# Kernel tuning notes

Hardware: AMD Instinct MI355X
Metric: run time of the kernel (lower is better)

## Reference

```python
import jax, jax.numpy as jnp
import numpy as np

D_MODEL, D_K, D_V, N_HEADS = 1024, 64, 64, 16
LN_EPS = 1e-5
NEG = -1e9

def setup_inputs() -> dict:
    key = jax.random.key(0)
    ks = jax.random.split(key, 8)
    B, S = 2, 2048
    inp = {
        'input_Q': jax.random.normal(ks[0], (B, S, D_MODEL), jnp.float32),
        'input_K': jax.random.normal(ks[1], (B, S, D_MODEL), jnp.float32),
        'input_V': jax.random.normal(ks[2], (B, S, D_MODEL), jnp.float32),
        'attn_mask': jax.random.randint(ks[3], (B, S, S), 0, 2).astype(bool),
    }
    sc = 1.0 / np.sqrt(D_MODEL)
    # weights stored as [in, out] so application is x @ W (matches torch Linear math)
    inp['W_Q'] = jax.random.uniform(ks[4], (D_MODEL, N_HEADS * D_K), jnp.float32, -sc, sc)
    inp['W_K'] = jax.random.uniform(ks[5], (D_MODEL, N_HEADS * D_K), jnp.float32, -sc, sc)
    inp['W_V'] = jax.random.uniform(ks[6], (D_MODEL, N_HEADS * D_V), jnp.float32, -sc, sc)
    inp['W_O'] = jax.random.uniform(ks[7], (N_HEADS * D_V, D_MODEL), jnp.float32, -sc, sc)
    return inp

def _mha(input_Q, input_K, input_V, attn_mask, W_Q, W_K, W_V, W_O):
    B, S, _ = input_Q.shape
    Q = (input_Q @ W_Q).reshape(B, S, N_HEADS, D_K).transpose(0, 2, 1, 3)  # [B,H,S,dk]
    K = (input_K @ W_K).reshape(B, S, N_HEADS, D_K).transpose(0, 2, 1, 3)
    V = (input_V @ W_V).reshape(B, S, N_HEADS, D_V).transpose(0, 2, 1, 3)
    scores = jnp.einsum('bhqd,bhkd->bhqk', Q, K) / np.sqrt(D_K)
    scores = jnp.where(attn_mask[:, None, :, :], NEG, scores)
    attn = jax.nn.softmax(scores, axis=-1)  # [B,H,S,S]
    context = jnp.einsum('bhqk,bhkd->bhqd', attn, V)
    context = context.transpose(0, 2, 1, 3).reshape(B, S, N_HEADS * D_V)
    output = context @ W_O
    y = output + input_Q  # residual
    # LayerNorm created fresh in forward: gamma=1, beta=0, eps=1e-5
    mu = jnp.mean(y, axis=-1, keepdims=True)
    var = jnp.mean((y - mu) ** 2, axis=-1, keepdims=True)
    out = (y - mu) / jnp.sqrt(var + LN_EPS)
    return out, attn

def reference(input_Q, input_K, input_V, attn_mask, W_Q, W_K, W_V, W_O):
    return _mha(input_Q, input_K, input_V, attn_mask, W_Q, W_K, W_V, W_O)
```

## Files before the change

### kernel.cpp

```cpp
#include <hip/hip_runtime.h>
#include <hip/hip_bf16.h>

typedef __attribute__((ext_vector_type(8))) short bf16x8;
typedef __attribute__((ext_vector_type(4))) float f32x4;

#define S 2048
#define DM 1024
#define NH 16
#define B_ 2

struct __align__(8) us4 { unsigned short a, b, c, d; };

static __device__ __forceinline__ unsigned short f2bf(float f) {
  unsigned int u = __builtin_bit_cast(unsigned int, f);
  u += 0x7fffu + ((u >> 16) & 1u);
  return (unsigned short)(u >> 16);
}

__global__ __launch_bounds__(256) void k_cvt(const float* __restrict__ x,
                                             unsigned short* __restrict__ y, int n) {
  int i = (blockIdx.x * 256 + threadIdx.x) * 4;
  if (i >= n) return;
  float4 v = *(const float4*)(x + i);
  us4 o; o.a = f2bf(v.x); o.b = f2bf(v.y); o.c = f2bf(v.z); o.d = f2bf(v.w);
  *(us4*)(y + i) = o;
}

__global__ __launch_bounds__(256) void k_wtr(const float* __restrict__ W,
                                             unsigned short* __restrict__ Wt) {
  __shared__ float tile[32][33];
  int n0 = blockIdx.x * 32, k0 = blockIdx.y * 32;
  int t = threadIdx.x;
  int r = t >> 3, c = (t & 7) * 4;
  float4 v = *(const float4*)(W + (long)(k0 + r) * DM + n0 + c);
  tile[r][c] = v.x; tile[r][c + 1] = v.y; tile[r][c + 2] = v.z; tile[r][c + 3] = v.w;
  __syncthreads();
  us4 o;
  o.a = f2bf(tile[c][r]); o.b = f2bf(tile[c + 1][r]);
  o.c = f2bf(tile[c + 2][r]); o.d = f2bf(tile[c + 3][r]);
  *(us4*)(Wt + (long)(n0 + r) * DM + k0 + c) = o;
}

template <int F32OUT>
__global__ __launch_bounds__(256) void k_gemm_nt(const unsigned short* __restrict__ A,
                                                 const unsigned short* __restrict__ Bt,
                                                 unsigned short* __restrict__ Cb,
                                                 float* __restrict__ Cf,
                                                 int M, int N, int K) {
  __shared__ unsigned short sA[128 * 40];
  __shared__ unsigned short sB[128 * 40];
  int t = threadIdx.x;
  int wave = t >> 6, lane = t & 63, quad = lane >> 4, l16 = lane & 15;
  int wm = (wave >> 1) * 64, wn = (wave & 1) * 64;
  long m0 = (long)blockIdx.x * 128, n0 = (long)blockIdx.y * 128;
  f32x4 acc[4][4] = {};
  int srow = t >> 1, sc = (t & 1) * 16;
  const unsigned short* Ag = A + (m0 + srow) * K + sc;
  const unsigned short* Bg = Bt + (n0 + srow) * K + sc;
  unsigned short* sAp = sA + srow * 40 + sc;
  unsigned short* sBp = sB + srow * 40 + sc;
  for (int k0 = 0; k0 < K; k0 += 32) {
    __syncthreads();
    int4 a0 = *(const int4*)(Ag + k0);
    int4 a1 = *(const int4*)(Ag + k0 + 8);
    int4 b0 = *(const int4*)(Bg + k0);
    int4 b1 = *(const int4*)(Bg + k0 + 8);
    *(int4*)(sAp) = a0; *(int4*)(sAp + 8) = a1;
    *(int4*)(sBp) = b0; *(int4*)(sBp + 8) = b1;
    __syncthreads();
    bf16x8 af[4], bfr[4];
#pragma unroll
    for (int i = 0; i < 4; i++) af[i] = *(const bf16x8*)(sA + (wm + i * 16 + l16) * 40 + quad * 8);
#pragma unroll
    for (int j = 0; j < 4; j++) bfr[j] = *(const bf16x8*)(sB + (wn + j * 16 + l16) * 40 + quad * 8);
#pragma unroll
    for (int i = 0; i < 4; i++)
#pragma unroll
      for (int j = 0; j < 4; j++)
        acc[i][j] = __builtin_amdgcn_mfma_f32_16x16x32_bf16(af[i], bfr[j], acc[i][j], 0, 0, 0);
  }
#pragma unroll
  for (int i = 0; i < 4; i++)
#pragma unroll
    for (int j = 0; j < 4; j++)
#pragma unroll
      for (int r = 0; r < 4; r++) {
        long row = m0 + wm + i * 16 + quad * 4 + r;
        long col = n0 + wn + j * 16 + l16;
        float v = acc[i][j][r];
        if (F32OUT) Cf[row * N + col] = v;
        else Cb[row * N + col] = f2bf(v);
      }
}

__global__ __launch_bounds__(256) void k_vtr(const unsigned short* __restrict__ Vp,
                                             unsigned short* __restrict__ Vt) {
  __shared__ unsigned short tile[64][72];
  int b = blockIdx.z, h = blockIdx.y, s0 = blockIdx.x * 64;
  int t = threadIdx.x;
  int r = t >> 2, c = (t & 3) * 16;
  const unsigned short* src = Vp + (long)(b * S + s0 + r) * DM + h * 64;
  *(int4*)(&tile[r][c]) = *(const int4*)(src + c);
  *(int4*)(&tile[r][c + 8]) = *(const int4*)(src + c + 8);
  __syncthreads();
  unsigned short o[16] __attribute__((aligned(16)));
#pragma unroll
  for (int i = 0; i < 16; i++) o[i] = tile[c + i][r];
  unsigned short* dst = Vt + ((long)(b * NH + h) * 64 + r) * S + s0 + c;
  *(int4*)(dst) = *(int4*)(o);
  *(int4*)(dst + 8) = *(int4*)(o + 8);
}

__global__ __launch_bounds__(256) void k_attn(const unsigned short* __restrict__ Qb,
                                              const unsigned short* __restrict__ Kb,
                                              const unsigned short* __restrict__ Vt,
                                              const int* __restrict__ mask,
                                              float* __restrict__ attn,
                                              unsigned short* __restrict__ ctx) {
  __shared__ unsigned short sQ[16 * 72];
  __shared__ unsigned short sK[128 * 72];
  __shared__ float sP[16 * 132];
  __shared__ float red[4][16];
  __shared__ float linv[16];
  int b = blockIdx.z, h = blockIdx.y, q0 = blockIdx.x * 16;
  int t = threadIdx.x;
  int wave = t >> 6, lane = t & 63, quad = lane >> 4, l16 = lane & 15;
  {
    int r = t >> 4, c = (t & 15) * 4;
    *(uint2*)(sQ + r * 72 + c) =
        *(const uint2*)(Qb + (long)(b * S + q0 + r) * DM + h * 64 + c);
  }
  const long mbase = (long)b * S * S;
  int krow = t >> 1, kc0 = (t & 1) * 32;
  const unsigned short* Kg = Kb + (long)(b * S + krow) * DM + h * 64 + kc0;
  unsigned short* sKp = sK + krow * 72 + kc0;

  float lsum[4] = {0.f, 0.f, 0.f, 0.f};
  for (int kt = 0; kt < 16; kt++) {
    __syncthreads();
    {
      const unsigned short* g = Kg + (long)kt * 128 * DM;
      *(int4*)(sKp) = *(const int4*)(g);
      *(int4*)(sKp + 8) = *(const int4*)(g + 8);
      *(int4*)(sKp + 16) = *(const int4*)(g + 16);
      *(int4*)(sKp + 24) = *(const int4*)(g + 24);
    }
    __syncthreads();
    bf16x8 aq0 = *(const bf16x8*)(sQ + l16 * 72 + quad * 8);
    bf16x8 aq1 = *(const bf16x8*)(sQ + l16 * 72 + 32 + quad * 8);
#pragma unroll
    for (int j = 0; j < 2; j++) {
      int kl = wave * 32 + j * 16 + l16;
      bf16x8 bk0 = *(const bf16x8*)(sK + kl * 72 + quad * 8);
      bf16x8 bk1 = *(const bf16x8*)(sK + kl * 72 + 32 + quad * 8);
      f32x4 fa = {0.f, 0.f, 0.f, 0.f};
      fa = __builtin_amdgcn_mfma_f32_16x16x32_bf16(aq0, bk0, fa, 0, 0, 0);
      fa = __builtin_amdgcn_mfma_f32_16x16x32_bf16(aq1, bk1, fa, 0, 0, 0);
      int colg = kt * 128 + kl;
#pragma unroll
      for (int r = 0; r < 4; r++) {
        int rowg = q0 + quad * 4 + r;
        int m = mask[mbase + (long)rowg * S + colg];
        float p = m ? 0.f : __expf(fa[r] * 0.125f);
        lsum[r] += p;
      }
    }
  }
#pragma unroll
  for (int r = 0; r < 4; r++)
    for (int off = 1; off < 16; off <<= 1) lsum[r] += __shfl_xor(lsum[r], off, 64);
  if (l16 == 0)
#pragma unroll
    for (int r = 0; r < 4; r++) red[wave][quad * 4 + r] = lsum[r];
  __syncthreads();
  if (t < 16) linv[t] = 1.f / (red[0][t] + red[1][t] + red[2][t] + red[3][t]);

  f32x4 oacc = {0.f, 0.f, 0.f, 0.f};
  const unsigned short* vbase = Vt + ((long)(b * NH + h) * 64 + wave * 16 + l16) * S;
  for (int kt = 0; kt < 16; kt++) {
    __syncthreads();
    {
      const unsigned short* g = Kg + (long)kt * 128 * DM;
      *(int4*)(sKp) = *(const int4*)(g);
      *(int4*)(sKp + 8) = *(const int4*)(g + 8);
      *(int4*)(sKp + 16) = *(const int4*)(g + 16);
      *(int4*)(sKp + 24) = *(const int4*)(g + 24);
    }
    __syncthreads();
    bf16x8 aq0 = *(const bf16x8*)(sQ + l16 * 72 + quad * 8);
    bf16x8 aq1 = *(const bf16x8*)(sQ + l16 * 72 + 32 + quad * 8);
#pragma unroll
    for (int j = 0; j < 2; j++) {
      int kl = wave * 32 + j * 16 + l16;
      bf16x8 bk0 = *(const bf16x8*)(sK + kl * 72 + quad * 8);
      bf16x8 bk1 = *(const bf16x8*)(sK + kl * 72 + 32 + quad * 8);
      f32x4 fa = {0.f, 0.f, 0.f, 0.f};
      fa = __builtin_amdgcn_mfma_f32_16x16x32_bf16(aq0, bk0, fa, 0, 0, 0);
      fa = __builtin_amdgcn_mfma_f32_16x16x32_bf16(aq1, bk1, fa, 0, 0, 0);
      int colg = kt * 128 + kl;
#pragma unroll
      for (int r = 0; r < 4; r++) {
        int rowg = q0 + quad * 4 + r;
        int m = mask[mbase + (long)rowg * S + colg];
        float p = m ? 0.f : __expf(fa[r] * 0.125f);
        sP[(quad * 4 + r) * 132 + wave * 32 + j * 16 + l16] = p;
      }
    }
    __syncthreads();
    {
      int r = t >> 4, c = (t & 15) * 8;
      float li = linv[r];
      const float* sp = sP + r * 132 + c;
      float4 v0 = *(const float4*)(sp);
      float4 v1 = *(const float4*)(sp + 4);
      v0.x *= li; v0.y *= li; v0.z *= li; v0.w *= li;
      v1.x *= li; v1.y *= li; v1.z *= li; v1.w *= li;
      float* dst = attn + ((long)(b * NH + h) * S + q0 + r) * S + kt * 128 + c;
      *(float4*)(dst) = v0;
      *(float4*)(dst + 4) = v1;
    }
#pragma unroll
    for (int ks = 0; ks < 4; ks++) {
      const float* ap = sP + l16 * 132 + ks * 32 + quad * 8;
      float4 a0 = *(const float4*)(ap);
      float4 a1 = *(const float4*)(ap + 4);
      bf16x8 a8;
      a8[0] = (short)f2bf(a0.x); a8[1] = (short)f2bf(a0.y);
      a8[2] = (short)f2bf(a0.z); a8[3] = (short)f2bf(a0.w);
      a8[4] = (short)f2bf(a1.x); a8[5] = (short)f2bf(a1.y);
      a8[6] = (short)f2bf(a1.z); a8[7] = (short)f2bf(a1.w);
      bf16x8 v8 = *(const bf16x8*)(vbase + kt * 128 + ks * 32 + quad * 8);
      oacc = __builtin_amdgcn_mfma_f32_16x16x32_bf16(a8, v8, oacc, 0, 0, 0);
    }
  }
#pragma unroll
  for (int r = 0; r < 4; r++) {
    int rowg = q0 + quad * 4 + r;
    float v = oacc[r] * linv[quad * 4 + r];
    ctx[((long)(b * S + rowg) * NH + h) * 64 + wave * 16 + l16] = f2bf(v);
  }
}

__global__ __launch_bounds__(256) void k_ln(const float* __restrict__ Y,
                                            const float* __restrict__ X,
                                            float* __restrict__ out) {
  __shared__ float rs[4], rs2[4];
  long row = blockIdx.x;
  int t = threadIdx.x;
  float4 v = *(const float4*)(Y + row * DM + t * 4);
  float4 xv = *(const float4*)(X + row * DM + t * 4);
  v.x += xv.x; v.y += xv.y; v.z += xv.z; v.w += xv.w;
  float s = v.x + v.y + v.z + v.w;
  float s2 = v.x * v.x + v.y * v.y + v.z * v.z + v.w * v.w;
  for (int off = 1; off < 64; off <<= 1) {
    s += __shfl_xor(s, off, 64);
    s2 += __shfl_xor(s2, off, 64);
  }
  int wave = t >> 6;
  if ((t & 63) == 0) { rs[wave] = s; rs2[wave] = s2; }
  __syncthreads();
  s = rs[0] + rs[1] + rs[2] + rs[3];
  s2 = rs2[0] + rs2[1] + rs2[2] + rs2[3];
  float mu = s * (1.f / 1024.f);
  float var = s2 * (1.f / 1024.f) - mu * mu;
  float rstd = rsqrtf(var + 1e-5f);
  float4 o;
  o.x = (v.x - mu) * rstd; o.y = (v.y - mu) * rstd;
  o.z = (v.z - mu) * rstd; o.w = (v.w - mu) * rstd;
  *(float4*)(out + row * DM + t * 4) = o;
}

extern "C" void kernel_launch(void* const* d_in, const int* in_sizes, int n_in,
                              void* d_out, int out_size, void* d_ws, size_t ws_size,
                              hipStream_t stream) {
  const float* inQ = (const float*)d_in[0];
  const float* inK = (const float*)d_in[1];
  const float* inV = (const float*)d_in[2];
  const int* mask = (const int*)d_in[3];
  const float* WQ = (const float*)d_in[4];
  const float* WK = (const float*)d_in[5];
  const float* WV = (const float*)d_in[6];
  const float* WO = (const float*)d_in[7];
  float* out = (float*)d_out;
  float* attn = out + (long)B_ * S * DM;

  char* ws = (char*)d_ws;
  const size_t MB = 1048576;
  unsigned short* WtQ = (unsigned short*)(ws + 0 * MB);
  unsigned short* WtK = (unsigned short*)(ws + 2 * MB);
  unsigned short* WtV = (unsigned short*)(ws + 4 * MB);
  unsigned short* WtO = (unsigned short*)(ws + 6 * MB);
  unsigned short* Xq = (unsigned short*)(ws + 8 * MB);
  unsigned short* Xk = (unsigned short*)(ws + 16 * MB);
  unsigned short* Xv = (unsigned short*)(ws + 24 * MB);
  unsigned short* Qb = (unsigned short*)(ws + 32 * MB);
  unsigned short* Kbf = (unsigned short*)(ws + 40 * MB);
  unsigned short* Vp = (unsigned short*)(ws + 48 * MB);
  unsigned short* Vtr = (unsigned short*)(ws + 56 * MB);
  unsigned short* ctx = (unsigned short*)(ws + 24 * MB);
  float* Yf = (float*)(ws + 8 * MB);

  dim3 blk(256);
  int n = B_ * S * DM;

  k_wtr<<<dim3(32, 32), blk, 0, stream>>>(WQ, WtQ);
  k_wtr<<<dim3(32, 32), blk, 0, stream>>>(WK, WtK);
  k_wtr<<<dim3(32, 32), blk, 0, stream>>>(WV, WtV);
  k_wtr<<<dim3(32, 32), blk, 0, stream>>>(WO, WtO);
  k_cvt<<<n / 1024, blk, 0, stream>>>(inQ, Xq, n);
  k_cvt<<<n / 1024, blk, 0, stream>>>(inK, Xk, n);
  k_cvt<<<n / 1024, blk, 0, stream>>>(inV, Xv, n);

  k_gemm_nt<0><<<dim3(32, 8), blk, 0, stream>>>(Xq, WtQ, Qb, nullptr, 4096, 1024, 1024);
  k_gemm_nt<0><<<dim3(32, 8), blk, 0, stream>>>(Xk, WtK, Kbf, nullptr, 4096, 1024, 1024);
  k_gemm_nt<0><<<dim3(32, 8), blk, 0, stream>>>(Xv, WtV, Vp, nullptr, 4096, 1024, 1024);

  k_vtr<<<dim3(32, 16, 2), blk, 0, stream>>>(Vp, Vtr);

  k_attn<<<dim3(128, 16, 2), blk, 0, stream>>>(Qb, Kbf, Vtr, mask, attn, ctx);

  k_gemm_nt<1><<<dim3(32, 8), blk, 0, stream>>>(ctx, WtO, nullptr, Yf, 4096, 1024, 1024);

  k_ln<<<B_ * S, blk, 0, stream>>>(Yf, inQ, out);
}
```

Before: 1.012 ms.

## Split attention into flash-style context kernel and tiled score-writer with bit-packed mask

Replaces the per-16-row attention kernel, which recomputed QK^T twice and read the int mask twice, with two kernels. A flash-style kernel accumulates row sums and P·V over 128-row query tiles and stores the inverse row sums. A separate 128x128 tiled kernel then recomputes the scores and writes the normalized attention matrix. The mask is first packed into bits with a ballot so the attention kernels read far less mask data. The GEMMs are also rewritten to use direct global-to-LDS loads with XOR swizzling, a K-step of 64 and 128x64 tiles. This adds a mask-packing pass and reuses workspace regions, which relies on the order of the stream.

```diff
diff --git a/kernel.cpp b/kernel.cpp
--- a/kernel.cpp
+++ b/kernel.cpp
@@ -15,6 +15,12 @@
   unsigned int u = __builtin_bit_cast(unsigned int, f);
   u += 0x7fffu + ((u >> 16) & 1u);
   return (unsigned short)(u >> 16);
+}
+
+typedef __attribute__((address_space(3))) unsigned int lds_u32;
+typedef __attribute__((address_space(1))) unsigned int gbl_u32;
+static __device__ __forceinline__ void gl_lds16(const unsigned short* g, short* l) {
+  __builtin_amdgcn_global_load_lds((gbl_u32*)(void*)g, (lds_u32*)l, 16, 0, 0);
 }
 
 __global__ __launch_bounds__(256) void k_cvt(const float* __restrict__ x,
@@ -41,48 +47,65 @@
   *(us4*)(Wt + (long)(n0 + r) * DM + k0 + c) = o;
 }
 
+__global__ __launch_bounds__(256) void k_pack(const int* __restrict__ mask,
+                                              unsigned int* __restrict__ bits) {
+  long gid = (long)blockIdx.x * 256 + threadIdx.x;
+  int m = mask[gid];
+  unsigned long long bm = __ballot(m != 0);
+  if ((threadIdx.x & 63) == 0) *(unsigned long long*)(bits + (gid >> 5)) = bm;
+}
+
 template <int F32OUT>
-__global__ __launch_bounds__(256) void k_gemm_nt(const unsigned short* __restrict__ A,
-                                                 const unsigned short* __restrict__ Bt,
-                                                 unsigned short* __restrict__ Cb,
-                                                 float* __restrict__ Cf,
-                                                 int M, int N, int K) {
-  __shared__ unsigned short sA[128 * 40];
-  __shared__ unsigned short sB[128 * 40];
+__global__ __launch_bounds__(256) void k_gemm2(const unsigned short* __restrict__ A,
+                                               const unsigned short* __restrict__ Bt,
+                                               unsigned short* __restrict__ Cb,
+                                               float* __restrict__ Cf,
+                                               int M, int N, int K) {
+  __shared__ __align__(16) char smem[24576];
+  short* sA = (short*)smem;
+  short* sB = (short*)(smem + 16384);
   int t = threadIdx.x;
   int wave = t >> 6, lane = t & 63, quad = lane >> 4, l16 = lane & 15;
-  int wm = (wave >> 1) * 64, wn = (wave & 1) * 64;
-  long m0 = (long)blockIdx.x * 128, n0 = (long)blockIdx.y * 128;
-  f32x4 acc[4][4] = {};
-  int srow = t >> 1, sc = (t & 1) * 16;
-  const unsigned short* Ag = A + (m0 + srow) * K + sc;
-  const unsigned short* Bg = Bt + (n0 + srow) * K + sc;
-  unsigned short* sAp = sA + srow * 40 + sc;
-  unsigned short* sBp = sB + srow * 40 + sc;
-  for (int k0 = 0; k0 < K; k0 += 32) {
+  int wm = (wave >> 1) * 64, wn = (wave & 1) * 32;
+  long m0 = (long)blockIdx.x * 128, n0 = (long)blockIdx.y * 64;
+  f32x4 acc[4][2] = {};
+  for (int k0 = 0; k0 < K; k0 += 64) {
     __syncthreads();
-    int4 a0 = *(const int4*)(Ag + k0);
-    int4 a1 = *(const int4*)(Ag + k0 + 8);
-    int4 b0 = *(const int4*)(Bg + k0);
-    int4 b1 = *(const int4*)(Bg + k0 + 8);
-    *(int4*)(sAp) = a0; *(int4*)(sAp + 8) = a1;
-    *(int4*)(sBp) = b0; *(int4*)(sBp + 8) = b1;
+#pragma unroll
+    for (int rr = 0; rr < 6; rr++) {
+      int id = rr * 4 + wave;
+      if (id < 16) {
+        int flat = id * 64 + lane;
+        int row = flat >> 3, cp = flat & 7, sw = cp ^ (row & 7);
+        gl_lds16(A + (m0 + row) * K + k0 + sw * 8, sA + id * 512);
+      } else {
+        int c = id - 16;
+        int flat = c * 64 + lane;
+        int row = flat >> 3, cp = flat & 7, sw = cp ^ (row & 7);
+        gl_lds16(Bt + (n0 + row) * K + k0 + sw * 8, sB + c * 512);
+      }
+    }
     __syncthreads();
-    bf16x8 af[4], bfr[4];
-#pragma unroll
-    for (int i = 0; i < 4; i++) af[i] = *(const bf16x8*)(sA + (wm + i * 16 + l16) * 40 + quad * 8);
-#pragma unroll
-    for (int j = 0; j < 4; j++) bfr[j] = *(const bf16x8*)(sB + (wn + j * 16 + l16) * 40 + quad * 8);
-#pragma unroll
-    for (int i = 0; i < 4; i++)
-#pragma unroll
-      for (int j = 0; j < 4; j++)
-        acc[i][j] = __builtin_amdgcn_mfma_f32_16x16x32_bf16(af[i], bfr[j], acc[i][j], 0, 0, 0);
+#pragma unroll
+    for (int kk = 0; kk < 2; kk++) {
+      bf16x8 af[4], bf_[2];
+#pragma unroll
+      for (int i = 0; i < 4; i++)
+        af[i] = *(const bf16x8*)(sA + (wm + i * 16 + l16) * 64 + (((kk * 4 + quad) ^ (l16 & 7)) * 8));
+#pragma unroll
+      for (int j = 0; j < 2; j++)
+        bf_[j] = *(const bf16x8*)(sB + (wn + j * 16 + l16) * 64 + (((kk * 4 + quad) ^ (l16 & 7)) * 8));
+#pragma unroll
+      for (int i = 0; i < 4; i++)
+#pragma unroll
+        for (int j = 0; j < 2; j++)
+          acc[i][j] = __builtin_amdgcn_mfma_f32_16x16x32_bf16(af[i], bf_[j], acc[i][j], 0, 0, 0);
+    }
   }
 #pragma unroll
   for (int i = 0; i < 4; i++)
 #pragma unroll
-    for (int j = 0; j < 4; j++)
+    for (int j = 0; j < 2; j++)
 #pragma unroll
       for (int r = 0; r < 4; r++) {
         long row = m0 + wm + i * 16 + quad * 4 + r;
@@ -111,134 +134,208 @@
   *(int4*)(dst + 8) = *(int4*)(o + 8);
 }
 
-__global__ __launch_bounds__(256) void k_attn(const unsigned short* __restrict__ Qb,
-                                              const unsigned short* __restrict__ Kb,
-                                              const unsigned short* __restrict__ Vt,
-                                              const int* __restrict__ mask,
-                                              float* __restrict__ attn,
-                                              unsigned short* __restrict__ ctx) {
-  __shared__ unsigned short sQ[16 * 72];
-  __shared__ unsigned short sK[128 * 72];
-  __shared__ float sP[16 * 132];
-  __shared__ float red[4][16];
-  __shared__ float linv[16];
-  int b = blockIdx.z, h = blockIdx.y, q0 = blockIdx.x * 16;
+__global__ __launch_bounds__(256) void k_flash(const unsigned short* __restrict__ Qb,
+                                               const unsigned short* __restrict__ Kb,
+                                               const unsigned short* __restrict__ Vt,
+                                               const unsigned int* __restrict__ mbits,
+                                               float* __restrict__ linvG,
+                                               unsigned short* __restrict__ ctx) {
+  __shared__ __align__(16) char smem[52736];
+  short* sP = (short*)smem;
+  short* sQ = (short*)(smem + 18432);
+  short* sK = (short*)(smem + 18432 + 16384);
+  short* sV = (short*)(smem + 18432 + 16384 + 8192);
+  unsigned long long* sM = (unsigned long long*)(smem + 18432 + 16384 + 8192 + 8192);
+  float* sLi = (float*)(smem + 18432 + 16384 + 8192 + 8192 + 1024);
+
+  const int b = blockIdx.z, h = blockIdx.y, q0 = blockIdx.x * 128;
+  const int bh = b * NH + h;
+  const int t = threadIdx.x;
+  const int wave = t >> 6, lane = t & 63, quad = lane >> 4, l16 = lane & 15;
+
+#pragma unroll
+  for (int rr = 0; rr < 4; rr++) {
+    int c = rr * 4 + wave;
+    int flat = c * 64 + lane;
+    int row = flat >> 3, cp = flat & 7, sw = cp ^ (row & 7);
+    gl_lds16(Qb + (long)(b * S + q0 + row) * DM + h * 64 + sw * 8, sQ + c * 512);
+  }
+  __syncthreads();
+  bf16x8 aq[2][2];
+#pragma unroll
+  for (int i = 0; i < 2; i++)
+#pragma unroll
+    for (int kk = 0; kk < 2; kk++)
+      aq[i][kk] = *(const bf16x8*)(sQ + (wave * 32 + i * 16 + l16) * 64 +
+                                   (((kk * 4 + quad) ^ (l16 & 7)) * 8));
+
+  f32x4 oacc[2][4] = {};
+  float lsum[2][4] = {};
+
+  for (int kt = 0; kt < 32; kt++) {
+    __syncthreads();
+#pragma unroll
+    for (int rr = 0; rr < 4; rr++) {
+      int id = rr * 4 + wave;
+      if (id < 8) {
+        int flat = id * 64 + lane;
+        int row = flat >> 3, cp = flat & 7, sw = cp ^ (row & 7);
+        gl_lds16(Kb + (long)(b * S + kt * 64 + row) * DM + h * 64 + sw * 8, sK + id * 512);
+      } else {
+        int cc = id - 8;
+        int flat = cc * 64 + lane;
+        int d = flat >> 3, cp = flat & 7, sw = cp ^ (d & 7);
+        gl_lds16(Vt + (long)(bh * 64 + d) * S + kt * 64 + sw * 8, sV + cc * 512);
+      }
+    }
+    if (t < 128)
+      sM[t] = *(const unsigned long long*)(mbits + ((long)(b * S) + q0 + t) * 64 + kt * 2);
+    __syncthreads();
+    f32x4 sacc[2][4] = {};
+#pragma unroll
+    for (int kk = 0; kk < 2; kk++) {
+      bf16x8 bk[4];
+#pragma unroll
+      for (int j = 0; j < 4; j++)
+        bk[j] = *(const bf16x8*)(sK + (j * 16 + l16) * 64 + (((kk * 4 + quad) ^ (l16 & 7)) * 8));
+#pragma unroll
+      for (int i = 0; i < 2; i++)
+#pragma unroll
+        for (int j = 0; j < 4; j++)
+          sacc[i][j] = __builtin_amdgcn_mfma_f32_16x16x32_bf16(aq[i][kk], bk[j], sacc[i][j], 0, 0, 0);
+    }
+#pragma unroll
+    for (int i = 0; i < 2; i++)
+#pragma unroll
+      for (int r = 0; r < 4; r++) {
+        int rl = wave * 32 + i * 16 + quad * 4 + r;
+        unsigned long long mw = sM[rl];
+        float ls = 0.f;
+#pragma unroll
+        for (int j = 0; j < 4; j++) {
+          int cb = j * 16 + l16;
+          float p = ((mw >> cb) & 1ull) ? 0.f : __expf(sacc[i][j][r] * 0.125f);
+          ls += p;
+          sP[rl * 72 + cb] = (short)f2bf(p);
+        }
+        lsum[i][r] += ls;
+      }
+    __syncthreads();
+#pragma unroll
+    for (int ks = 0; ks < 2; ks++) {
+      bf16x8 aP[2], bV[4];
+#pragma unroll
+      for (int i = 0; i < 2; i++)
+        aP[i] = *(const bf16x8*)(sP + (wave * 32 + i * 16 + l16) * 72 + ks * 32 + quad * 8);
+#pragma unroll
+      for (int j = 0; j < 4; j++)
+        bV[j] = *(const bf16x8*)(sV + (j * 16 + l16) * 64 + (((ks * 4 + quad) ^ (l16 & 7)) * 8));
+#pragma unroll
+      for (int i = 0; i < 2; i++)
+#pragma unroll
+        for (int j = 0; j < 4; j++)
+          oacc[i][j] = __builtin_amdgcn_mfma_f32_16x16x32_bf16(aP[i], bV[j], oacc[i][j], 0, 0, 0);
+    }
+  }
+#pragma unroll
+  for (int i = 0; i < 2; i++)
+#pragma unroll
+    for (int r = 0; r < 4; r++) {
+      float v = lsum[i][r];
+      for (int off = 1; off < 16; off <<= 1) v += __shfl_xor(v, off, 64);
+      if (l16 == 0) {
+        int rl = wave * 32 + i * 16 + quad * 4 + r;
+        float li = 1.f / v;
+        sLi[rl] = li;
+        linvG[(long)bh * S + q0 + rl] = li;
+      }
+    }
+  __syncthreads();
+#pragma unroll
+  for (int i = 0; i < 2; i++)
+#pragma unroll
+    for (int r = 0; r < 4; r++) {
+      int rl = wave * 32 + i * 16 + quad * 4 + r;
+      float li = sLi[rl];
+#pragma unroll
+      for (int j = 0; j < 4; j++) {
+        float v = oacc[i][j][r] * li;
+        ctx[((long)(b * S + q0 + rl) * NH + h) * 64 + j * 16 + l16] = f2bf(v);
+      }
+    }
+}
+
+__global__ __launch_bounds__(256) void k_score(const unsigned short* __restrict__ Qb,
+                                               const unsigned short* __restrict__ Kb,
+                                               const unsigned int* __restrict__ mbits,
+                                               const float* __restrict__ linvG,
+                                               float* __restrict__ attn) {
+  __shared__ __align__(16) char smem[35328];
+  short* sQ = (short*)smem;
+  short* sK = (short*)(smem + 16384);
+  unsigned long long* sM = (unsigned long long*)(smem + 32768);
+  float* sLi = (float*)(smem + 32768 + 2048);
+  int q0 = blockIdx.x * 128, k0 = blockIdx.y * 128, bh = blockIdx.z;
+  int b = bh >> 4, h = bh & 15;
   int t = threadIdx.x;
   int wave = t >> 6, lane = t & 63, quad = lane >> 4, l16 = lane & 15;
+  int wq = wave >> 1, wk = wave & 1;
+#pragma unroll
+  for (int rr = 0; rr < 8; rr++) {
+    int id = rr * 4 + wave;
+    if (id < 16) {
+      int flat = id * 64 + lane;
+      int row = flat >> 3, cp = flat & 7, sw = cp ^ (row & 7);
+      gl_lds16(Qb + (long)(b * S + q0 + row) * DM + h * 64 + sw * 8, sQ + id * 512);
+    } else {
+      int c = id - 16;
+      int flat = c * 64 + lane;
+      int row = flat >> 3, cp = flat & 7, sw = cp ^ (row & 7);
+      gl_lds16(Kb + (long)(b * S + k0 + row) * DM + h * 64 + sw * 8, sK + c * 512);
+    }
+  }
   {
-    int r = t >> 4, c = (t & 15) * 4;
-    *(uint2*)(sQ + r * 72 + c) =
-        *(const uint2*)(Qb + (long)(b * S + q0 + r) * DM + h * 64 + c);
-  }
-  const long mbase = (long)b * S * S;
-  int krow = t >> 1, kc0 = (t & 1) * 32;
-  const unsigned short* Kg = Kb + (long)(b * S + krow) * DM + h * 64 + kc0;
-  unsigned short* sKp = sK + krow * 72 + kc0;
-
-  float lsum[4] = {0.f, 0.f, 0.f, 0.f};
-  for (int kt = 0; kt < 16; kt++) {
-    __syncthreads();
-    {
-      const unsigned short* g = Kg + (long)kt * 128 * DM;
-      *(int4*)(sKp) = *(const int4*)(g);
-      *(int4*)(sKp + 8) = *(const int4*)(g + 8);
-      *(int4*)(sKp + 16) = *(const int4*)(g + 16);
-      *(int4*)(sKp + 24) = *(const int4*)(g + 24);
-    }
-    __syncthreads();
-    bf16x8 aq0 = *(const bf16x8*)(sQ + l16 * 72 + quad * 8);
-    bf16x8 aq1 = *(const bf16x8*)(sQ + l16 * 72 + 32 + quad * 8);
-#pragma unroll
-    for (int j = 0; j < 2; j++) {
-      int kl = wave * 32 + j * 16 + l16;
-      bf16x8 bk0 = *(const bf16x8*)(sK + kl * 72 + quad * 8);
-      bf16x8 bk1 = *(const bf16x8*)(sK + kl * 72 + 32 + quad * 8);
-      f32x4 fa = {0.f, 0.f, 0.f, 0.f};
-      fa = __builtin_amdgcn_mfma_f32_16x16x32_bf16(aq0, bk0, fa, 0, 0, 0);
-      fa = __builtin_amdgcn_mfma_f32_16x16x32_bf16(aq1, bk1, fa, 0, 0, 0);
-      int colg = kt * 128 + kl;
-#pragma unroll
-      for (int r = 0; r < 4; r++) {
-        int rowg = q0 + quad * 4 + r;
-        int m = mask[mbase + (long)rowg * S + colg];
-        float p = m ? 0.f : __expf(fa[r] * 0.125f);
-        lsum[r] += p;
-      }
-    }
-  }
-#pragma unroll
-  for (int r = 0; r < 4; r++)
-    for (int off = 1; off < 16; off <<= 1) lsum[r] += __shfl_xor(lsum[r], off, 64);
-  if (l16 == 0)
-#pragma unroll
-    for (int r = 0; r < 4; r++) red[wave][quad * 4 + r] = lsum[r];
-  __syncthreads();
-  if (t < 16) linv[t] = 1.f / (red[0][t] + red[1][t] + red[2][t] + red[3][t]);
-
-  f32x4 oacc = {0.f, 0.f, 0.f, 0.f};
-  const unsigned short* vbase = Vt + ((long)(b * NH + h) * 64 + wave * 16 + l16) * S;
-  for (int kt = 0; kt < 16; kt++) {
-    __syncthreads();
-    {
-      const unsigned short* g = Kg + (long)kt * 128 * DM;
-      *(int4*)(sKp) = *(const int4*)(g);
-      *(int4*)(sKp + 8) = *(const int4*)(g + 8);
-      *(int4*)(sKp + 16) = *(const int4*)(g + 16);
-      *(int4*)(sKp + 24) = *(const int4*)(g + 24);
-    }
-    __syncthreads();
-    bf16x8 aq0 = *(const bf16x8*)(sQ + l16 * 72 + quad * 8);
-    bf16x8 aq1 = *(const bf16x8*)(sQ + l16 * 72 + 32 + quad * 8);
-#pragma unroll
-    for (int j = 0; j < 2; j++) {
-      int kl = wave * 32 + j * 16 + l16;
-      bf16x8 bk0 = *(const bf16x8*)(sK + kl * 72 + quad * 8);
-      bf16x8 bk1 = *(const bf16x8*)(sK + kl * 72 + 32 + quad * 8);
-      f32x4 fa = {0.f, 0.f, 0.f, 0.f};
-      fa = __builtin_amdgcn_mfma_f32_16x16x32_bf16(aq0, bk0, fa, 0, 0, 0);
-      fa = __builtin_amdgcn_mfma_f32_16x16x32_bf16(aq1, bk1, fa, 0, 0, 0);
-      int colg = kt * 128 + kl;
-#pragma unroll
-      for (int r = 0; r < 4; r++) {
-        int rowg = q0 + quad * 4 + r;
-        int m = mask[mbase + (long)rowg * S + colg];
-        float p = m ? 0.f : __expf(fa[r] * 0.125f);
-        sP[(quad * 4 + r) * 132 + wave * 32 + j * 16 + l16] = p;
-      }
-    }
-    __syncthreads();
-    {
-      int r = t >> 4, c = (t & 15) * 8;
-      float li = linv[r];
-      const float* sp = sP + r * 132 + c;
-      float4 v0 = *(const float4*)(sp);
-      float4 v1 = *(const float4*)(sp + 4);
-      v0.x *= li; v0.y *= li; v0.z *= li; v0.w *= li;
-      v1.x *= li; v1.y *= li; v1.z *= li; v1.w *= li;
-      float* dst = attn + ((long)(b * NH + h) * S + q0 + r) * S + kt * 128 + c;
-      *(float4*)(dst) = v0;
-      *(float4*)(dst + 4) = v1;
-    }
-#pragma unroll
-    for (int ks = 0; ks < 4; ks++) {
-      const float* ap = sP + l16 * 132 + ks * 32 + quad * 8;
-      float4 a0 = *(const float4*)(ap);
-      float4 a1 = *(const float4*)(ap + 4);
-      bf16x8 a8;
-      a8[0] = (short)f2bf(a0.x); a8[1] = (short)f2bf(a0.y);
-      a8[2] = (short)f2bf(a0.z); a8[3] = (short)f2bf(a0.w);
-      a8[4] = (short)f2bf(a1.x); a8[5] = (short)f2bf(a1.y);
-      a8[6] = (short)f2bf(a1.z); a8[7] = (short)f2bf(a1.w);
-      bf16x8 v8 = *(const bf16x8*)(vbase + kt * 128 + ks * 32 + quad * 8);
-      oacc = __builtin_amdgcn_mfma_f32_16x16x32_bf16(a8, v8, oacc, 0, 0, 0);
-    }
-  }
-#pragma unroll
-  for (int r = 0; r < 4; r++) {
-    int rowg = q0 + quad * 4 + r;
-    float v = oacc[r] * linv[quad * 4 + r];
-    ctx[((long)(b * S + rowg) * NH + h) * 64 + wave * 16 + l16] = f2bf(v);
-  }
+    int row = t >> 1, half = t & 1;
+    sM[row * 2 + half] =
+        *(const unsigned long long*)(mbits + ((long)(b * S) + q0 + row) * 64 + (k0 >> 5) + half * 2);
+  }
+  if (t < 128) sLi[t] = linvG[(long)bh * S + q0 + t];
+  __syncthreads();
+  bf16x8 a_[4][2], b_[4][2];
+#pragma unroll
+  for (int i = 0; i < 4; i++)
+#pragma unroll
+    for (int kk = 0; kk < 2; kk++)
+      a_[i][kk] = *(const bf16x8*)(sQ + (wq * 64 + i * 16 + l16) * 64 +
+                                   (((kk * 4 + quad) ^ (l16 & 7)) * 8));
+#pragma unroll
+  for (int j = 0; j < 4; j++)
+#pragma unroll
+    for (int kk = 0; kk < 2; kk++)
+      b_[j][kk] = *(const bf16x8*)(sK + (wk * 64 + j * 16 + l16) * 64 +
+                                   (((kk * 4 + quad) ^ (l16 & 7)) * 8));
+  f32x4 sacc[4][4] = {};
+#pragma unroll
+  for (int kk = 0; kk < 2; kk++)
+#pragma unroll
+    for (int i = 0; i < 4; i++)
+#pragma unroll
+      for (int j = 0; j < 4; j++)
+        sacc[i][j] = __builtin_amdgcn_mfma_f32_16x16x32_bf16(a_[i][kk], b_[j][kk], sacc[i][j], 0, 0, 0);
+#pragma unroll
+  for (int i = 0; i < 4; i++)
+#pragma unroll
+    for (int r = 0; r < 4; r++) {
+      int rl = wq * 64 + i * 16 + quad * 4 + r;
+      unsigned long long mw = sM[rl * 2 + wk];
+      float li = sLi[rl];
+      float* dst = attn + ((long)bh * S + q0 + rl) * S + k0 + wk * 64;
+#pragma unroll
+      for (int j = 0; j < 4; j++) {
+        float p = ((mw >> (j * 16 + l16)) & 1ull) ? 0.f : __expf(sacc[i][j][r] * 0.125f) * li;
+        dst[j * 16 + l16] = p;
+      }
+    }
 }
 
 __global__ __launch_bounds__(256) void k_ln(const float* __restrict__ Y,
@@ -297,6 +394,8 @@
   unsigned short* Kbf = (unsigned short*)(ws + 40 * MB);
   unsigned short* Vp = (unsigned short*)(ws + 48 * MB);
   unsigned short* Vtr = (unsigned short*)(ws + 56 * MB);
+  unsigned int* mbits = (unsigned int*)(ws + 48 * MB);
+  float* linvG = (float*)(ws + 50 * MB);
   unsigned short* ctx = (unsigned short*)(ws + 24 * MB);
   float* Yf = (float*)(ws + 8 * MB);
 
@@ -311,15 +410,17 @@
   k_cvt<<<n / 1024, blk, 0, stream>>>(inK, Xk, n);
   k_cvt<<<n / 1024, blk, 0, stream>>>(inV, Xv, n);
 
-  k_gemm_nt<0><<<dim3(32, 8), blk, 0, stream>>>(Xq, WtQ, Qb, nullptr, 4096, 1024, 1024);
-  k_gemm_nt<0><<<dim3(32, 8), blk, 0, stream>>>(Xk, WtK, Kbf, nullptr, 4096, 1024, 1024);
-  k_gemm_nt<0><<<dim3(32, 8), blk, 0, stream>>>(Xv, WtV, Vp, nullptr, 4096, 1024, 1024);
+  k_gemm2<0><<<dim3(32, 16), blk, 0, stream>>>(Xq, WtQ, Qb, nullptr, 4096, 1024, 1024);
+  k_gemm2<0><<<dim3(32, 16), blk, 0, stream>>>(Xk, WtK, Kbf, nullptr, 4096, 1024, 1024);
+  k_gemm2<0><<<dim3(32, 16), blk, 0, stream>>>(Xv, WtV, Vp, nullptr, 4096, 1024, 1024);
 
   k_vtr<<<dim3(32, 16, 2), blk, 0, stream>>>(Vp, Vtr);
-
-  k_attn<<<dim3(128, 16, 2), blk, 0, stream>>>(Qb, Kbf, Vtr, mask, attn, ctx);
-
-  k_gemm_nt<1><<<dim3(32, 8), blk, 0, stream>>>(ctx, WtO, nullptr, Yf, 4096, 1024, 1024);
+  k_pack<<<dim3((B_ * S * S) / 256), blk, 0, stream>>>(mask, mbits);
+
+  k_flash<<<dim3(16, 16, 2), blk, 0, stream>>>(Qb, Kbf, Vtr, mbits, linvG, ctx);
+  k_score<<<dim3(16, 16, 32), blk, 0, stream>>>(Qb, Kbf, mbits, linvG, attn);
+
+  k_gemm2<1><<<dim3(32, 16), blk, 0, stream>>>(ctx, WtO, nullptr, Yf, 4096, 1024, 1024);
 
   k_ln<<<B_ * S, blk, 0, stream>>>(Yf, inQ, out);
 }
```

Result: faster. 821.8 us (-18.8%).
